# Performance work log

Measured on AMD Instinct MI355X. Metric: run time of the kernel, lower is better.

## Reference

```python
import jax, jax.numpy as jnp
import numpy as np

N_POINTS = 500_000
D_PHASE = 6
N_BINS = 128
LO, HI = -4.0, 4.0


def setup_inputs() -> dict:
    key = jax.random.key(0)
    x = jax.random.normal(key, (N_POINTS, D_PHASE), dtype=jnp.float32)
    edges_x = jnp.linspace(LO, HI, N_BINS + 1, dtype=jnp.float32)
    edges_y = jnp.linspace(LO, HI, N_BINS + 1, dtype=jnp.float32)
    return {"x": x, "edges_x": edges_x, "edges_y": edges_y}


def reference(x, edges_x, edges_y):
    # Histogram2D(axis=(0,1), bandwidth=(1.0,1.0), kde=True).forward(x)
    # bin centers from edges
    cx = 0.5 * (edges_x[:-1] + edges_x[1:])  # (nx,)
    cy = 0.5 * (edges_y[:-1] + edges_y[1:])  # (ny,)
    # resolution = first bin width; bandwidth = 1.0 * resolution
    bwx = edges_x[1] - edges_x[0]
    bwy = edges_y[1] - edges_y[0]
    # per-point Gaussian kernel evaluations against bin centers
    kx = jnp.exp(-0.5 * jnp.square((x[:, 0][:, None] - cx[None, :]) / bwx))  # (n, nx)
    ky = jnp.exp(-0.5 * jnp.square((x[:, 1][:, None] - cy[None, :]) / bwy))  # (n, ny)
    # accumulate joint KDE histogram via outer-product contraction over points
    hist = jnp.einsum("ni,nj->ij", kx, ky)  # (nx, ny)
    # normalize to a probability density (integrates to 1 over the grid)
    hist = hist / (jnp.sum(hist) * bwx * bwy)
    return hist
```

## Files before the change

kernel.cpp:

```cpp
#include <hip/hip_runtime.h>

#define NBINS 128
#define NB2   (NBINS * NBINS)
#define TPB   1024
#define NBLK  256
#define KC    32
#define NTEAM 4
#define ROWB  (KC * 2)

typedef __attribute__((ext_vector_type(8)))  short short8;
typedef __attribute__((ext_vector_type(16))) float f32x16;

__device__ __forceinline__ float exp2_fast(float x) {
#if defined(__has_builtin)
#if __has_builtin(__builtin_amdgcn_exp2f)
    return __builtin_amdgcn_exp2f(x);
#else
    return exp2f(x);
#endif
#else
    return exp2f(x);
#endif
}

__device__ __forceinline__ unsigned pk_bf16(float a, float b) {
    const unsigned ar = __float_as_uint(a) + 0x8000u;
    const unsigned br = __float_as_uint(b) + 0x8000u;
    return __builtin_amdgcn_perm(br, ar, 0x07060302u);
}

#define WC (-0.72134752044448170f)
#define E1 (0.36787944117144233f)

union __align__(16) ShMem {
    struct {
        unsigned short tiles[2][NTEAM][2][NBINS][KC];
        float uv[2][NTEAM][2][KC];
    } s;
    float hist[NB2];
};

__global__ __launch_bounds__(TPB, 4) void kde_mfma_kernel(
    const float* __restrict__ x,
    const float* __restrict__ ex,
    const float* __restrict__ ey,
    float* __restrict__ out,
    int n, int nchunks)
{
    __shared__ ShMem sm;

    const int tid  = (int)threadIdx.x;
    const int lane = tid & 63;
    const int half = lane >> 5;
    const int l31  = lane & 31;
    const int w4   = (tid >> 6) & 3;
    const int team = tid >> 8;
    const int rowblk = (w4 >> 1) * 64;
    const int colblk = (w4 & 1) * 64;

    const float lox = ex[0], loy = ey[0];
    const float ibx = 1.0f / (ex[1] - ex[0]);
    const float iby = 1.0f / (ey[1] - ey[0]);

    const int tt     = tid & 255;
    const int pI     = tt & 15;
    const int dimi   = (tt >> 4) & 1;
    const int eighth = tt >> 5;
    const float cc   = (float)(eighth * 16 + 8);

    f32x16 acc[2][2];
    #pragma unroll
    for (int a = 0; a < 2; ++a)
        #pragma unroll
        for (int c = 0; c < 2; ++c)
            #pragma unroll
            for (int r = 0; r < 16; ++r) acc[a][c][r] = 0.f;

    const int niter = (nchunks + NBLK * NTEAM - 1) / (NBLK * NTEAM);

    auto stage = [&](int jt) {
        if (tid < NTEAM * KC && jt < niter) {
            const int tm = tid >> 5, idx = tid & 31;
            const int g  = (int)blockIdx.x * NTEAM + tm + jt * (NBLK * NTEAM);
            if (g < nchunks) {
                const int p = g * KC + idx;
                float uu = 1e9f, vv = 1e9f;
                if (p < n) {
                    const float2 xy = *(const float2*)(x + (size_t)p * 6);
                    uu = (xy.x - lox) * ibx - 0.5f;
                    vv = (xy.y - loy) * iby - 0.5f;
                }
                sm.s.uv[jt & 1][tm][0][idx] = uu;
                sm.s.uv[jt & 1][tm][1][idx] = vv;
            }
        }
    };

    auto gen = [&](int jt) {
        const int g = (int)blockIdx.x * NTEAM + team + jt * (NBLK * NTEAM);
        if (g >= nchunks) return;
        const int bb = jt & 1;
        const float* uvp = sm.s.uv[bb][team][dimi];
        const float u0 = uvp[2 * pI], u1 = uvp[2 * pI + 1];
        const float d0 = fminf(fmaxf(u0 - cc, -88.f), 88.f);
        const float d1 = fminf(fmaxf(u1 - cc, -88.f), 88.f);
        const float w0 = exp2_fast((WC * d0) * d0);
        const float w1 = exp2_fast((WC * d1) * d1);
        float r0 = exp2_fast(fmaf(-2.f * WC, d0, WC));
        float r1 = exp2_fast(fmaf(-2.f * WC, d1, WC));
        float q0 = exp2_fast(fmaf( 2.f * WC, d0, WC));
        float q1 = exp2_fast(fmaf( 2.f * WC, d1, WC));
        char* tb0 = (char*)&sm.s.tiles[bb][team][dimi][0][0]
                  + (eighth * 16 + 8) * ROWB;
        const int o0 = pI << 2;
        const int os[4] = { o0, o0 ^ 16, o0 ^ 32, o0 ^ 48 };
        float a0 = w0, a1 = w1;
        #pragma unroll
        for (int j = 0; j < 8; ++j) {
            *(unsigned*)(tb0 + j * ROWB + os[j & 3]) = pk_bf16(a0, a1);
            a0 *= r0; r0 *= E1;
            a1 *= r1; r1 *= E1;
        }
        a0 = w0; a1 = w1;
        #pragma unroll
        for (int j = 1; j <= 8; ++j) {
            a0 *= q0; a1 *= q1;
            *(unsigned*)(tb0 - j * ROWB + os[(4 - j) & 3]) = pk_bf16(a0, a1);
            q0 *= E1; q1 *= E1;
        }
    };

    auto domfma = [&](int it) {
        const int g = (int)blockIdx.x * NTEAM + team + it * (NBLK * NTEAM);
        if (g >= nchunks) return;
        const int bb = it & 1;
        const char* Ab = (const char*)&sm.s.tiles[bb][team][0][0][0];
        const char* Bb = (const char*)&sm.s.tiles[bb][team][1][0][0];
        const int ra = rowblk + l31, ca = colblk + l31;
        const int swa = (ra & 3) << 4, swb = (ca & 3) << 4;
        #pragma unroll
        for (int s4 = 0; s4 < 2; ++s4) {
            const int kb2 = s4 * 32 + half * 16;
            const short8 a0 = *(const short8*)(Ab + ra * ROWB        + (kb2 ^ swa));
            const short8 a1 = *(const short8*)(Ab + (ra + 32) * ROWB + (kb2 ^ swa));
            const short8 b0 = *(const short8*)(Bb + ca * ROWB        + (kb2 ^ swb));
            const short8 b1 = *(const short8*)(Bb + (ca + 32) * ROWB + (kb2 ^ swb));
            acc[0][0] = __builtin_amdgcn_mfma_f32_32x32x16_bf16(a0, b0, acc[0][0], 0, 0, 0);
            acc[0][1] = __builtin_amdgcn_mfma_f32_32x32x16_bf16(a0, b1, acc[0][1], 0, 0, 0);
            acc[1][0] = __builtin_amdgcn_mfma_f32_32x32x16_bf16(a1, b0, acc[1][0], 0, 0, 0);
            acc[1][1] = __builtin_amdgcn_mfma_f32_32x32x16_bf16(a1, b1, acc[1][1], 0, 0, 0);
        }
    };

    stage(0);
    __syncthreads();
    stage(1);
    gen(0);
    __syncthreads();
    for (int it = 0; it < niter; ++it) {
        stage(it + 2);
        domfma(it);
        gen(it + 1);
        __syncthreads();
    }

    for (int tm = 0; tm < NTEAM; ++tm) {
        if (team == tm) {
            #pragma unroll
            for (int rb = 0; rb < 2; ++rb)
                #pragma unroll
                for (int tj = 0; tj < 2; ++tj)
                    #pragma unroll
                    for (int r = 0; r < 16; ++r) {
                        const int row = rowblk + rb * 32 + (r & 3) + 8 * (r >> 2) + 4 * half;
                        const int col = colblk + tj * 32 + l31;
                        const int a = row * NBINS + col;
                        const float v = acc[rb][tj][r];
                        if (tm == 0) sm.hist[a] = v;
                        else         sm.hist[a] += v;
                    }
        }
        __syncthreads();
    }

    for (int i = tid; i < NB2; i += TPB)
        unsafeAtomicAdd(&out[i], sm.hist[i]);
}

__global__ __launch_bounds__(TPB) void kde_final_kernel(
    float* __restrict__ out,
    const float* __restrict__ ex,
    const float* __restrict__ ey)
{
    __shared__ float red[TPB / 64];
    __shared__ float sinv;
    const int tid = (int)threadIdx.x;

    float4 v[4];
    float s = 0.f;
    #pragma unroll
    for (int i = 0; i < 4; ++i) {
        v[i] = ((const float4*)out)[tid + i * TPB];
        s += v[i].x + v[i].y + v[i].z + v[i].w;
    }
    #pragma unroll
    for (int off = 32; off > 0; off >>= 1) s += __shfl_down(s, off, 64);
    if ((tid & 63) == 0) red[tid >> 6] = s;
    __syncthreads();
    if (tid == 0) {
        float t = 0.f;
        #pragma unroll
        for (int i = 0; i < TPB / 64; ++i) t += red[i];
        sinv = 1.0f / (t * (ex[1] - ex[0]) * (ey[1] - ey[0]));
    }
    __syncthreads();
    const float inv = sinv;
    #pragma unroll
    for (int i = 0; i < 4; ++i) {
        float4 o = v[i];
        o.x *= inv; o.y *= inv; o.z *= inv; o.w *= inv;
        ((float4*)out)[tid + i * TPB] = o;
    }
}

extern "C" void kernel_launch(void* const* d_in, const int* in_sizes, int n_in,
                              void* d_out, int out_size, void* d_ws, size_t ws_size,
                              hipStream_t stream)
{
    const float* x  = (const float*)d_in[0];
    const float* ex = (const float*)d_in[1];
    const float* ey = (const float*)d_in[2];
    float* out = (float*)d_out;
    const int n = in_sizes[0] / 6;
    const int nchunks = (n + KC - 1) / KC;

    hipMemsetAsync(d_out, 0, NB2 * sizeof(float), stream);
    kde_mfma_kernel<<<NBLK, TPB, 0, stream>>>(x, ex, ey, out, n, nchunks);
    kde_final_kernel<<<1, TPB, 0, stream>>>(out, ex, ey);
}
```

Measured before the change: 110.7 us.

## Fuse normalization into main kernel via last-block epilogue and interleave LDS tiles

Drops the separate normalization kernel. Each block reduces its accumulator sum into a workspace float with an atomic, and the last block to finish (found with an atomic counter) rescales the output histogram in place. The shared-memory tile layout also changes so the x and y kernel rows for each bin are interleaved in a 128-byte row, with an 8-way XOR swizzle. This removes one kernel launch and the global re-read of the histogram, at the cost of an extra memset, serialized tail work in one block, and the total sum now coming from the per-block accumulators.

After: 169.5 us. +53.1%, slower.

```diff
diff --git a/kernel.cpp b/kernel.cpp
--- a/kernel.cpp
+++ b/kernel.cpp
@@ -6,7 +6,7 @@
 #define NBLK  256
 #define KC    32
 #define NTEAM 4
-#define ROWB  (KC * 2)
+#define ROWB  128
 
 typedef __attribute__((ext_vector_type(8)))  short short8;
 typedef __attribute__((ext_vector_type(16))) float f32x16;
@@ -34,7 +34,7 @@
 
 union __align__(16) ShMem {
     struct {
-        unsigned short tiles[2][NTEAM][2][NBINS][KC];
+        unsigned short tiles[2][NTEAM][NBINS][2][KC];
         float uv[2][NTEAM][2][KC];
     } s;
     float hist[NB2];
@@ -45,9 +45,12 @@
     const float* __restrict__ ex,
     const float* __restrict__ ey,
     float* __restrict__ out,
+    unsigned* __restrict__ ws,
     int n, int nchunks)
 {
     __shared__ ShMem sm;
+    __shared__ float wred[TPB / 64];
+    __shared__ unsigned s_old;
 
     const int tid  = (int)threadIdx.x;
     const int lane = tid & 63;
@@ -66,7 +69,9 @@
     const int pI     = tt & 15;
     const int dimi   = (tt >> 4) & 1;
     const int eighth = tt >> 5;
-    const float cc   = (float)(eighth * 16 + 8);
+    const int cI     = eighth * 16 + 8;
+    const float cc   = (float)cI;
+    const int dimbase = dimi * 64 + pI * 4;
 
     f32x16 acc[2][2];
     #pragma unroll
@@ -110,22 +115,23 @@
         float r1 = exp2_fast(fmaf(-2.f * WC, d1, WC));
         float q0 = exp2_fast(fmaf( 2.f * WC, d0, WC));
         float q1 = exp2_fast(fmaf( 2.f * WC, d1, WC));
-        char* tb0 = (char*)&sm.s.tiles[bb][team][dimi][0][0]
-                  + (eighth * 16 + 8) * ROWB;
-        const int o0 = pI << 2;
-        const int os[4] = { o0, o0 ^ 16, o0 ^ 32, o0 ^ 48 };
+        char* tb = (char*)&sm.s.tiles[bb][team][0][0][0];
         float a0 = w0, a1 = w1;
         #pragma unroll
         for (int j = 0; j < 8; ++j) {
-            *(unsigned*)(tb0 + j * ROWB + os[j & 3]) = pk_bf16(a0, a1);
+            const int row = cI + j;
+            *(unsigned*)(tb + row * ROWB + (dimbase ^ ((row & 7) << 4))) =
+                pk_bf16(a0, a1);
             a0 *= r0; r0 *= E1;
             a1 *= r1; r1 *= E1;
         }
         a0 = w0; a1 = w1;
         #pragma unroll
         for (int j = 1; j <= 8; ++j) {
+            const int row = cI - j;
             a0 *= q0; a1 *= q1;
-            *(unsigned*)(tb0 - j * ROWB + os[(4 - j) & 3]) = pk_bf16(a0, a1);
+            *(unsigned*)(tb + row * ROWB + (dimbase ^ ((row & 7) << 4))) =
+                pk_bf16(a0, a1);
             q0 *= E1; q1 *= E1;
         }
     };
@@ -134,17 +140,16 @@
         const int g = (int)blockIdx.x * NTEAM + team + it * (NBLK * NTEAM);
         if (g >= nchunks) return;
         const int bb = it & 1;
-        const char* Ab = (const char*)&sm.s.tiles[bb][team][0][0][0];
-        const char* Bb = (const char*)&sm.s.tiles[bb][team][1][0][0];
+        const char* tb = (const char*)&sm.s.tiles[bb][team][0][0][0];
         const int ra = rowblk + l31, ca = colblk + l31;
-        const int swa = (ra & 3) << 4, swb = (ca & 3) << 4;
+        const int sa = (ra & 7) << 4, sb = (ca & 7) << 4;
         #pragma unroll
         for (int s4 = 0; s4 < 2; ++s4) {
             const int kb2 = s4 * 32 + half * 16;
-            const short8 a0 = *(const short8*)(Ab + ra * ROWB        + (kb2 ^ swa));
-            const short8 a1 = *(const short8*)(Ab + (ra + 32) * ROWB + (kb2 ^ swa));
-            const short8 b0 = *(const short8*)(Bb + ca * ROWB        + (kb2 ^ swb));
-            const short8 b1 = *(const short8*)(Bb + (ca + 32) * ROWB + (kb2 ^ swb));
+            const short8 a0 = *(const short8*)(tb + ra * ROWB        + ( kb2       ^ sa));
+            const short8 a1 = *(const short8*)(tb + (ra + 32) * ROWB + ( kb2       ^ sa));
+            const short8 b0 = *(const short8*)(tb + ca * ROWB        + ((kb2 + 64) ^ sb));
+            const short8 b1 = *(const short8*)(tb + (ca + 32) * ROWB + ((kb2 + 64) ^ sb));
             acc[0][0] = __builtin_amdgcn_mfma_f32_32x32x16_bf16(a0, b0, acc[0][0], 0, 0, 0);
             acc[0][1] = __builtin_amdgcn_mfma_f32_32x32x16_bf16(a0, b1, acc[0][1], 0, 0, 0);
             acc[1][0] = __builtin_amdgcn_mfma_f32_32x32x16_bf16(a1, b0, acc[1][0], 0, 0, 0);
@@ -162,6 +167,24 @@
         domfma(it);
         gen(it + 1);
         __syncthreads();
+    }
+
+    float ts = 0.f;
+    #pragma unroll
+    for (int rb = 0; rb < 2; ++rb)
+        #pragma unroll
+        for (int tj = 0; tj < 2; ++tj)
+            #pragma unroll
+            for (int r = 0; r < 16; ++r) ts += acc[rb][tj][r];
+    #pragma unroll
+    for (int off = 32; off > 0; off >>= 1) ts += __shfl_down(ts, off, 64);
+    if (lane == 0) wred[tid >> 6] = ts;
+    __syncthreads();
+    if (tid == 0) {
+        float bs = 0.f;
+        #pragma unroll
+        for (int i = 0; i < TPB / 64; ++i) bs += wred[i];
+        unsafeAtomicAdd((float*)&ws[1], bs);
     }
 
     for (int tm = 0; tm < NTEAM; ++tm) {
@@ -185,41 +208,22 @@
 
     for (int i = tid; i < NB2; i += TPB)
         unsafeAtomicAdd(&out[i], sm.hist[i]);
-}
-
-__global__ __launch_bounds__(TPB) void kde_final_kernel(
-    float* __restrict__ out,
-    const float* __restrict__ ex,
-    const float* __restrict__ ey)
-{
-    __shared__ float red[TPB / 64];
-    __shared__ float sinv;
-    const int tid = (int)threadIdx.x;
-
-    float4 v[4];
-    float s = 0.f;
-    #pragma unroll
-    for (int i = 0; i < 4; ++i) {
-        v[i] = ((const float4*)out)[tid + i * TPB];
-        s += v[i].x + v[i].y + v[i].z + v[i].w;
-    }
-    #pragma unroll
-    for (int off = 32; off > 0; off >>= 1) s += __shfl_down(s, off, 64);
-    if ((tid & 63) == 0) red[tid >> 6] = s;
-    __syncthreads();
-    if (tid == 0) {
-        float t = 0.f;
-        #pragma unroll
-        for (int i = 0; i < TPB / 64; ++i) t += red[i];
-        sinv = 1.0f / (t * (ex[1] - ex[0]) * (ey[1] - ey[0]));
-    }
-    __syncthreads();
-    const float inv = sinv;
-    #pragma unroll
-    for (int i = 0; i < 4; ++i) {
-        float4 o = v[i];
-        o.x *= inv; o.y *= inv; o.z *= inv; o.w *= inv;
-        ((float4*)out)[tid + i * TPB] = o;
+
+    __threadfence();
+    __syncthreads();
+    if (tid == 0) s_old = atomicAdd(&ws[0], 1u);
+    __syncthreads();
+    if (s_old == NBLK - 1) {
+        __threadfence();
+        const float sum = __hip_atomic_load((const float*)&ws[1],
+                                            __ATOMIC_RELAXED,
+                                            __HIP_MEMORY_SCOPE_AGENT);
+        const float inv = ibx * iby / sum;
+        for (int i = tid; i < NB2; i += TPB) {
+            const float v = __hip_atomic_load(&out[i], __ATOMIC_RELAXED,
+                                              __HIP_MEMORY_SCOPE_AGENT);
+            out[i] = v * inv;
+        }
     }
 }
 
@@ -235,6 +239,7 @@
     const int nchunks = (n + KC - 1) / KC;
 
     hipMemsetAsync(d_out, 0, NB2 * sizeof(float), stream);
-    kde_mfma_kernel<<<NBLK, TPB, 0, stream>>>(x, ex, ey, out, n, nchunks);
-    kde_final_kernel<<<1, TPB, 0, stream>>>(out, ex, ey);
-}
+    hipMemsetAsync(d_ws, 0, 2 * sizeof(unsigned), stream);
+    kde_mfma_kernel<<<NBLK, TPB, 0, stream>>>(x, ex, ey, out,
+                                              (unsigned*)d_ws, n, nchunks);
+}
```

## Use single-team 256-thread blocks with direct atomic reduction of accumulators

Applied to the files above, without the earlier changes.

Restructures the KDE kernel from 256 blocks of 1024 threads (four teams sharing a block) into 1024 blocks of 256 threads, each block one team. The in-block shared-memory reduction across teams is dropped, and every wave atomically adds its MFMA accumulators straight to global memory. The point load is split so the global read is issued before the MFMA work and written to LDS after generation, hiding load latency. This removes the cross-team reduction and its barriers, but quadruples the number of global atomics per output bin and makes the grid smaller-grained.

New measurement: 140.8 us. 27.2% more time.

```diff
diff --git a/kernel.cpp b/kernel.cpp
--- a/kernel.cpp
+++ b/kernel.cpp
@@ -2,11 +2,10 @@
 
 #define NBINS 128
 #define NB2   (NBINS * NBINS)
-#define TPB   1024
-#define NBLK  256
+#define TPB   256
+#define NBLK  1024
 #define KC    32
-#define NTEAM 4
-#define ROWB  (KC * 2)
+#define DIMSH 4128
 
 typedef __attribute__((ext_vector_type(8)))  short short8;
 typedef __attribute__((ext_vector_type(16))) float f32x16;
@@ -32,14 +31,6 @@
 #define WC (-0.72134752044448170f)
 #define E1 (0.36787944117144233f)
 
-union __align__(16) ShMem {
-    struct {
-        unsigned short tiles[2][NTEAM][2][NBINS][KC];
-        float uv[2][NTEAM][2][KC];
-    } s;
-    float hist[NB2];
-};
-
 __global__ __launch_bounds__(TPB, 4) void kde_mfma_kernel(
     const float* __restrict__ x,
     const float* __restrict__ ex,
@@ -47,14 +38,14 @@
     float* __restrict__ out,
     int n, int nchunks)
 {
-    __shared__ ShMem sm;
+    __shared__ unsigned short tiles[2][2][DIMSH];
+    __shared__ float uv[2][2][KC];
 
     const int tid  = (int)threadIdx.x;
     const int lane = tid & 63;
     const int half = lane >> 5;
     const int l31  = lane & 31;
-    const int w4   = (tid >> 6) & 3;
-    const int team = tid >> 8;
+    const int w4   = tid >> 6;
     const int rowblk = (w4 >> 1) * 64;
     const int colblk = (w4 & 1) * 64;
 
@@ -62,11 +53,11 @@
     const float ibx = 1.0f / (ex[1] - ex[0]);
     const float iby = 1.0f / (ey[1] - ey[0]);
 
-    const int tt     = tid & 255;
-    const int pI     = tt & 15;
-    const int dimi   = (tt >> 4) & 1;
-    const int eighth = tt >> 5;
-    const float cc   = (float)(eighth * 16 + 8);
+    const int pI     = tid & 15;
+    const int dimi   = (tid >> 4) & 1;
+    const int eighth = tid >> 5;
+    const int cI     = eighth * 16 + 8;
+    const float cc   = (float)cI;
 
     f32x16 acc[2][2];
     #pragma unroll
@@ -76,31 +67,33 @@
             #pragma unroll
             for (int r = 0; r < 16; ++r) acc[a][c][r] = 0.f;
 
-    const int niter = (nchunks + NBLK * NTEAM - 1) / (NBLK * NTEAM);
-
-    auto stage = [&](int jt) {
-        if (tid < NTEAM * KC && jt < niter) {
-            const int tm = tid >> 5, idx = tid & 31;
-            const int g  = (int)blockIdx.x * NTEAM + tm + jt * (NBLK * NTEAM);
+    const int niter = (nchunks + NBLK - 1) / NBLK;
+
+    float2 xy; bool ldv = false;
+    auto ld_xy = [&](int jt) {
+        ldv = false;
+        if (tid < KC && jt < niter) {
+            const int g = (int)blockIdx.x + jt * NBLK;
             if (g < nchunks) {
-                const int p = g * KC + idx;
-                float uu = 1e9f, vv = 1e9f;
-                if (p < n) {
-                    const float2 xy = *(const float2*)(x + (size_t)p * 6);
-                    uu = (xy.x - lox) * ibx - 0.5f;
-                    vv = (xy.y - loy) * iby - 0.5f;
-                }
-                sm.s.uv[jt & 1][tm][0][idx] = uu;
-                sm.s.uv[jt & 1][tm][1][idx] = vv;
+                ldv = true;
+                const int p = g * KC + tid;
+                if (p < n) xy = *(const float2*)(x + (size_t)p * 6);
+                else       xy = make_float2(3e9f, 3e9f);
             }
         }
     };
+    auto write_uv = [&](int jt) {
+        if (ldv) {
+            uv[jt & 1][0][tid] = (xy.x - lox) * ibx - 0.5f;
+            uv[jt & 1][1][tid] = (xy.y - loy) * iby - 0.5f;
+        }
+    };
 
     auto gen = [&](int jt) {
-        const int g = (int)blockIdx.x * NTEAM + team + jt * (NBLK * NTEAM);
+        const int g = (int)blockIdx.x + jt * NBLK;
         if (g >= nchunks) return;
         const int bb = jt & 1;
-        const float* uvp = sm.s.uv[bb][team][dimi];
+        const float* uvp = uv[bb][dimi];
         const float u0 = uvp[2 * pI], u1 = uvp[2 * pI + 1];
         const float d0 = fminf(fmaxf(u0 - cc, -88.f), 88.f);
         const float d1 = fminf(fmaxf(u1 - cc, -88.f), 88.f);
@@ -110,14 +103,13 @@
         float r1 = exp2_fast(fmaf(-2.f * WC, d1, WC));
         float q0 = exp2_fast(fmaf( 2.f * WC, d0, WC));
         float q1 = exp2_fast(fmaf( 2.f * WC, d1, WC));
-        char* tb0 = (char*)&sm.s.tiles[bb][team][dimi][0][0]
-                  + (eighth * 16 + 8) * ROWB;
+        char* tb0 = (char*)&tiles[bb][dimi][0] + cI * 64;
         const int o0 = pI << 2;
         const int os[4] = { o0, o0 ^ 16, o0 ^ 32, o0 ^ 48 };
         float a0 = w0, a1 = w1;
         #pragma unroll
         for (int j = 0; j < 8; ++j) {
-            *(unsigned*)(tb0 + j * ROWB + os[j & 3]) = pk_bf16(a0, a1);
+            *(unsigned*)(tb0 + j * 64 + os[j & 3]) = pk_bf16(a0, a1);
             a0 *= r0; r0 *= E1;
             a1 *= r1; r1 *= E1;
         }
@@ -125,26 +117,26 @@
         #pragma unroll
         for (int j = 1; j <= 8; ++j) {
             a0 *= q0; a1 *= q1;
-            *(unsigned*)(tb0 - j * ROWB + os[(4 - j) & 3]) = pk_bf16(a0, a1);
+            *(unsigned*)(tb0 - j * 64 + os[(4 - j) & 3]) = pk_bf16(a0, a1);
             q0 *= E1; q1 *= E1;
         }
     };
 
     auto domfma = [&](int it) {
-        const int g = (int)blockIdx.x * NTEAM + team + it * (NBLK * NTEAM);
+        const int g = (int)blockIdx.x + it * NBLK;
         if (g >= nchunks) return;
         const int bb = it & 1;
-        const char* Ab = (const char*)&sm.s.tiles[bb][team][0][0][0];
-        const char* Bb = (const char*)&sm.s.tiles[bb][team][1][0][0];
+        const char* Ab = (const char*)&tiles[bb][0][0];
+        const char* Bb = (const char*)&tiles[bb][1][0];
         const int ra = rowblk + l31, ca = colblk + l31;
-        const int swa = (ra & 3) << 4, swb = (ca & 3) << 4;
+        const int sa = (ra & 3) << 4, sb = (ca & 3) << 4;
         #pragma unroll
         for (int s4 = 0; s4 < 2; ++s4) {
             const int kb2 = s4 * 32 + half * 16;
-            const short8 a0 = *(const short8*)(Ab + ra * ROWB        + (kb2 ^ swa));
-            const short8 a1 = *(const short8*)(Ab + (ra + 32) * ROWB + (kb2 ^ swa));
-            const short8 b0 = *(const short8*)(Bb + ca * ROWB        + (kb2 ^ swb));
-            const short8 b1 = *(const short8*)(Bb + (ca + 32) * ROWB + (kb2 ^ swb));
+            const short8 a0 = *(const short8*)(Ab + ra * 64        + (kb2 ^ sa));
+            const short8 a1 = *(const short8*)(Ab + (ra + 32) * 64 + (kb2 ^ sa));
+            const short8 b0 = *(const short8*)(Bb + ca * 64        + (kb2 ^ sb));
+            const short8 b1 = *(const short8*)(Bb + (ca + 32) * 64 + (kb2 ^ sb));
             acc[0][0] = __builtin_amdgcn_mfma_f32_32x32x16_bf16(a0, b0, acc[0][0], 0, 0, 0);
             acc[0][1] = __builtin_amdgcn_mfma_f32_32x32x16_bf16(a0, b1, acc[0][1], 0, 0, 0);
             acc[1][0] = __builtin_amdgcn_mfma_f32_32x32x16_bf16(a1, b0, acc[1][0], 0, 0, 0);
@@ -152,47 +144,36 @@
         }
     };
 
-    stage(0);
-    __syncthreads();
-    stage(1);
-    gen(0);
+    ld_xy(0); write_uv(0);
+    __syncthreads();
+    ld_xy(1); gen(0); write_uv(1);
     __syncthreads();
     for (int it = 0; it < niter; ++it) {
-        stage(it + 2);
+        ld_xy(it + 2);
         domfma(it);
         gen(it + 1);
+        write_uv(it + 2);
         __syncthreads();
     }
 
-    for (int tm = 0; tm < NTEAM; ++tm) {
-        if (team == tm) {
+    #pragma unroll
+    for (int rb = 0; rb < 2; ++rb)
+        #pragma unroll
+        for (int tj = 0; tj < 2; ++tj)
             #pragma unroll
-            for (int rb = 0; rb < 2; ++rb)
-                #pragma unroll
-                for (int tj = 0; tj < 2; ++tj)
-                    #pragma unroll
-                    for (int r = 0; r < 16; ++r) {
-                        const int row = rowblk + rb * 32 + (r & 3) + 8 * (r >> 2) + 4 * half;
-                        const int col = colblk + tj * 32 + l31;
-                        const int a = row * NBINS + col;
-                        const float v = acc[rb][tj][r];
-                        if (tm == 0) sm.hist[a] = v;
-                        else         sm.hist[a] += v;
-                    }
-        }
-        __syncthreads();
-    }
-
-    for (int i = tid; i < NB2; i += TPB)
-        unsafeAtomicAdd(&out[i], sm.hist[i]);
-}
-
-__global__ __launch_bounds__(TPB) void kde_final_kernel(
+            for (int r = 0; r < 16; ++r) {
+                const int row = rowblk + rb * 32 + (r & 3) + 8 * (r >> 2) + 4 * half;
+                const int col = colblk + tj * 32 + l31;
+                unsafeAtomicAdd(&out[row * NBINS + col], acc[rb][tj][r]);
+            }
+}
+
+__global__ __launch_bounds__(1024) void kde_final_kernel(
     float* __restrict__ out,
     const float* __restrict__ ex,
     const float* __restrict__ ey)
 {
-    __shared__ float red[TPB / 64];
+    __shared__ float red[1024 / 64];
     __shared__ float sinv;
     const int tid = (int)threadIdx.x;
 
@@ -200,7 +181,7 @@
     float s = 0.f;
     #pragma unroll
     for (int i = 0; i < 4; ++i) {
-        v[i] = ((const float4*)out)[tid + i * TPB];
+        v[i] = ((const float4*)out)[tid + i * 1024];
         s += v[i].x + v[i].y + v[i].z + v[i].w;
     }
     #pragma unroll
@@ -210,7 +191,7 @@
     if (tid == 0) {
         float t = 0.f;
         #pragma unroll
-        for (int i = 0; i < TPB / 64; ++i) t += red[i];
+        for (int i = 0; i < 1024 / 64; ++i) t += red[i];
         sinv = 1.0f / (t * (ex[1] - ex[0]) * (ey[1] - ey[0]));
     }
     __syncthreads();
@@ -219,7 +200,7 @@
     for (int i = 0; i < 4; ++i) {
         float4 o = v[i];
         o.x *= inv; o.y *= inv; o.z *= inv; o.w *= inv;
-        ((float4*)out)[tid + i * TPB] = o;
+        ((float4*)out)[tid + i * 1024] = o;
     }
 }
 
@@ -236,5 +217,5 @@
 
     hipMemsetAsync(d_out, 0, NB2 * sizeof(float), stream);
     kde_mfma_kernel<<<NBLK, TPB, 0, stream>>>(x, ex, ey, out, n, nchunks);
-    kde_final_kernel<<<1, TPB, 0, stream>>>(out, ex, ey);
-}
+    kde_final_kernel<<<1, 1024, 0, stream>>>(out, ex, ey);
+}
```
